# Kernel optimization log

Measured on AMD Instinct MI355X. Metric: run time of the kernel, lower is better.

The kernel has to match this reference:

```python
import jax, jax.numpy as jnp
import numpy as np

N_NODES = 50000
N_EDGES = 800000
FEAT_DIM = 64


def setup_inputs() -> dict:
    key = jax.random.key(0)
    k1, k2, k3 = jax.random.split(key, 3)
    x = jax.random.normal(k1, (N_NODES, FEAT_DIM), dtype=jnp.float32)
    beta = jnp.ones((1,), dtype=jnp.float32)
    # CSR-equivalent edge list: sorted destination rows + random source columns
    row_index = jnp.sort(jax.random.randint(k2, (N_EDGES,), 0, N_NODES, dtype=jnp.int32))
    col_index = jax.random.randint(k3, (N_EDGES,), 0, N_NODES, dtype=jnp.int32)
    return {"x": x, "beta": beta, "row_index": row_index, "col_index": col_index}


def reference(x, beta, row_index, col_index):
    """AGNN layer: SDDMM edge attention (beta * cosine similarity) over the
    sparse graph, per-row softmax, then sparse neighbor aggregation.
    Equivalent math to mygraph.SDDMM + mygraph.agnn_udf (select_id == 5).
    x: [N, D]; row_index/col_index: [E] edge endpoints (row = destination).
    """
    N = x.shape[0]
    eps = 1e-8
    # L2-normalize node features for cosine similarity
    xn = x * jax.lax.rsqrt(jnp.sum(x * x, axis=-1, keepdims=True) + eps)  # [N, D]
    # SDDMM: attention only on existing edges
    att = beta[0] * jnp.sum(xn[row_index] * xn[col_index], axis=-1)  # [E]
    # Numerically stable segment softmax over each destination row
    m = jax.ops.segment_max(att, row_index, num_segments=N)  # [N]
    m = jnp.where(jnp.isfinite(m), m, 0.0)  # empty rows -> -inf guard
    e = jnp.exp(att - m[row_index])  # [E]
    denom = jax.ops.segment_sum(e, row_index, num_segments=N)  # [N]
    alpha = e / jnp.maximum(denom[row_index], 1e-16)  # [E]
    # Sparse aggregation: out_i = sum_j alpha_ij * x_j
    out = jax.ops.segment_sum(alpha[:, None] * x[col_index], row_index, num_segments=N)
    return out
```

## Files before the change

kernel.cpp:

```cpp
#include <hip/hip_runtime.h>
#include <hip/hip_bf16.h>

#define FEAT 64

__global__ void prep_kernel(const float* __restrict__ x,
                            float* __restrict__ rn,
                            const int* __restrict__ row,
                            int* __restrict__ row_ptr,
                            int N, int E, int normBlocks) {
    if ((int)blockIdx.x < normBlocks) {
        int wid  = blockIdx.x * (blockDim.x >> 6) + (threadIdx.x >> 6);
        int lane = threadIdx.x & 63;
        int g    = lane >> 3;
        int sub  = lane & 7;
        int r    = wid * 8 + g;
        if (r >= N) return;
        const char* xB = (const char*)x;
        uint roff = ((uint)r << 8) + ((uint)sub << 4);
        float4 xa = *reinterpret_cast<const float4*>(xB + roff);
        float4 xb = *reinterpret_cast<const float4*>(xB + roff + 128);
        float q = xa.x*xa.x + xa.y*xa.y + xa.z*xa.z + xa.w*xa.w
                + xb.x*xb.x + xb.y*xb.y + xb.z*xb.z + xb.w*xb.w;
        q += __shfl_xor(q, 1);
        q += __shfl_xor(q, 2);
        q += __shfl_xor(q, 4);
        if (sub == 0) rn[r] = rsqrtf(q + 1e-8f);
    } else {
        int e = (blockIdx.x - normBlocks) * blockDim.x + threadIdx.x;
        if (e >= E) return;
        int curr = row[e];
        if (e == 0) {
            for (int r = 0; r <= curr; ++r) row_ptr[r] = 0;
        } else {
            int prev = row[e - 1];
            for (int r = prev + 1; r <= curr; ++r) row_ptr[r] = e;
        }
        if (e == E - 1) {
            for (int r = curr + 1; r <= N; ++r) row_ptr[r] = E;
        }
    }
}

__global__ void fused_kernel(const float* __restrict__ x,
                             const float* __restrict__ rn,
                             const float* __restrict__ beta,
                             const int* __restrict__ row_ptr,
                             const int* __restrict__ col,
                             float* __restrict__ out, int N) {
    int wid  = blockIdx.x * (blockDim.x >> 6) + (threadIdx.x >> 6);
    int lane = threadIdx.x & 63;
    int g    = lane >> 3;
    int sub  = lane & 7;
    int r    = wid * 8 + g;
    bool rv  = (r < N);

    int start = 0, deg = 0;
    if (rv) {
        start = row_ptr[r];
        deg   = row_ptr[r + 1] - start;
    }

    const char* xB   = (const char*)x;
    uint        subo = (uint)sub << 4;

    int   cols8 = 0;
    float rns8  = 0.f;
    if (sub < deg) {
        cols8 = col[start + sub];
        rns8  = rn[cols8];
    }

    float4 xa = make_float4(0.f, 0.f, 0.f, 0.f);
    float4 xb = make_float4(0.f, 0.f, 0.f, 0.f);
    if (rv) {
        uint roff = ((uint)r << 8) + subo;
        xa = *reinterpret_cast<const float4*>(xB + roff);
        xb = *reinterpret_cast<const float4*>(xB + roff + 128);
        float brn = beta[0] * rn[r];
        xa.x *= brn; xa.y *= brn; xa.z *= brn; xa.w *= brn;
        xb.x *= brn; xb.y *= brn; xb.z *= brn; xb.w *= brn;
    }

    float  s = 0.f;
    float4 aa = make_float4(0.f, 0.f, 0.f, 0.f);
    float4 ab = make_float4(0.f, 0.f, 0.f, 0.f);

    for (int k = 0; k < deg; k += 2) {
        int kk = k & 7;
        if (k && kk == 0) {
            if (k + sub < deg) {
                cols8 = col[start + k + sub];
                rns8  = rn[cols8];
            }
        }
        int   c0  = __shfl(cols8, kk, 8);
        float rn0 = __shfl(rns8,  kk, 8);
        int   c1  = __shfl(cols8, kk + 1, 8);
        float rn1 = __shfl(rns8,  kk + 1, 8);
        bool  v1  = (k + 1) < deg;

        uint o0 = ((uint)c0 << 8) + subo;
        float4 va0 = *reinterpret_cast<const float4*>(xB + o0);
        float4 vb0 = *reinterpret_cast<const float4*>(xB + o0 + 128);
        float4 va1 = make_float4(0.f, 0.f, 0.f, 0.f);
        float4 vb1 = make_float4(0.f, 0.f, 0.f, 0.f);
        if (v1) {
            uint o1 = ((uint)c1 << 8) + subo;
            va1 = *reinterpret_cast<const float4*>(xB + o1);
            vb1 = *reinterpret_cast<const float4*>(xB + o1 + 128);
        }

        float d0 = xa.x*va0.x + xa.y*va0.y + xa.z*va0.z + xa.w*va0.w
                 + xb.x*vb0.x + xb.y*vb0.y + xb.z*vb0.z + xb.w*vb0.w;
        float d1 = xa.x*va1.x + xa.y*va1.y + xa.z*va1.z + xa.w*va1.w
                 + xb.x*vb1.x + xb.y*vb1.y + xb.z*vb1.z + xb.w*vb1.w;
        d0 += __shfl_xor(d0, 1);  d1 += __shfl_xor(d1, 1);
        d0 += __shfl_xor(d0, 2);  d1 += __shfl_xor(d1, 2);
        d0 += __shfl_xor(d0, 4);  d1 += __shfl_xor(d1, 4);

        float e0 = __expf(d0 * rn0);
        float e1 = v1 ? __expf(d1 * rn1) : 0.f;
        s += e0 + e1;

        aa.x += e0 * va0.x + e1 * va1.x;  aa.y += e0 * va0.y + e1 * va1.y;
        aa.z += e0 * va0.z + e1 * va1.z;  aa.w += e0 * va0.w + e1 * va1.w;
        ab.x += e0 * vb0.x + e1 * vb1.x;  ab.y += e0 * vb0.y + e1 * vb1.y;
        ab.z += e0 * vb0.z + e1 * vb1.z;  ab.w += e0 * vb0.w + e1 * vb1.w;
    }

    float inv = 1.0f / fmaxf(s, 1e-16f);
    if (rv) {
        uint roff = ((uint)r << 8) + subo;
        *reinterpret_cast<float4*>((char*)out + roff) =
            make_float4(aa.x * inv, aa.y * inv, aa.z * inv, aa.w * inv);
        *reinterpret_cast<float4*>((char*)out + roff + 128) =
            make_float4(ab.x * inv, ab.y * inv, ab.z * inv, ab.w * inv);
    }
}

extern "C" void kernel_launch(void* const* d_in, const int* in_sizes, int n_in,
                              void* d_out, int out_size, void* d_ws, size_t ws_size,
                              hipStream_t stream) {
    const float* x    = (const float*)d_in[0];
    const float* beta = (const float*)d_in[1];
    const int*   row  = (const int*)d_in[2];
    const int*   col  = (const int*)d_in[3];
    float*       out  = (float*)d_out;

    const int N = in_sizes[0] / FEAT;
    const int E = in_sizes[2];

    float* rn      = (float*)d_ws;
    int*   row_ptr = (int*)(rn + ((N + 63) & ~63));

    {
        int normBlocks = (N + 31) / 32;
        int edgeBlocks = (E + 255) / 256;
        prep_kernel<<<normBlocks + edgeBlocks, 256, 0, stream>>>(
            x, rn, row, row_ptr, N, E, normBlocks);
    }
    {
        int waves = (N + 7) / 8;
        int grid  = (waves + 3) / 4;
        fused_kernel<<<grid, 256, 0, stream>>>(x, rn, beta, row_ptr, col, out, N);
    }
}
```

Baseline: 41.71 us.

## Gather bf16 normalized features and assign one wave per row

The prep kernel now also writes a bf16 copy of the L2-normalized features plus each row's norm. The fused kernel gathers these 128-byte bf16 rows instead of 256-byte fp32 rows and rescales by the norm to rebuild x for aggregation, halving gather traffic. Work moves from eight rows per wave to one row per wave, with each 8-lane group taking a different neighbor. Column indices are software-prefetched two chunks ahead and partials are reduced across groups at the end. This adds a workspace buffer and extra prep writes, and bf16 rounding lowers the precision of both the attention scores and the aggregated values.

Measured after the change: 43.35 us. +3.9%, slower.

```diff
diff --git a/kernel.cpp b/kernel.cpp
--- a/kernel.cpp
+++ b/kernel.cpp
@@ -3,8 +3,28 @@
 
 #define FEAT 64
 
+__device__ inline uint packbf2(float lo, float hi) {
+    uint ul = __float_as_uint(lo), uh = __float_as_uint(hi);
+    ul += 0x7FFFu + ((ul >> 16) & 1u);
+    uh += 0x7FFFu + ((uh >> 16) & 1u);
+    return (ul >> 16) | (uh & 0xFFFF0000u);
+}
+
+__device__ inline void unpack8(uint4 q, float4& va, float4& vb) {
+    va.x = __uint_as_float(q.x << 16);
+    va.y = __uint_as_float(q.x & 0xFFFF0000u);
+    va.z = __uint_as_float(q.y << 16);
+    va.w = __uint_as_float(q.y & 0xFFFF0000u);
+    vb.x = __uint_as_float(q.z << 16);
+    vb.y = __uint_as_float(q.z & 0xFFFF0000u);
+    vb.z = __uint_as_float(q.w << 16);
+    vb.w = __uint_as_float(q.w & 0xFFFF0000u);
+}
+
 __global__ void prep_kernel(const float* __restrict__ x,
                             float* __restrict__ rn,
+                            float* __restrict__ nrm,
+                            uint4* __restrict__ xhn,
                             const int* __restrict__ row,
                             int* __restrict__ row_ptr,
                             int N, int E, int normBlocks) {
@@ -24,7 +44,15 @@
         q += __shfl_xor(q, 1);
         q += __shfl_xor(q, 2);
         q += __shfl_xor(q, 4);
-        if (sub == 0) rn[r] = rsqrtf(q + 1e-8f);
+        float qe  = q + 1e-8f;
+        float rnr = rsqrtf(qe);
+        if (sub == 0) { rn[r] = rnr; nrm[r] = qe * rnr; }
+        uint4 p;
+        p.x = packbf2(xa.x * rnr, xa.y * rnr);
+        p.y = packbf2(xa.z * rnr, xa.w * rnr);
+        p.z = packbf2(xb.x * rnr, xb.y * rnr);
+        p.w = packbf2(xb.z * rnr, xb.w * rnr);
+        xhn[r * 8 + sub] = p;
     } else {
         int e = (blockIdx.x - normBlocks) * blockDim.x + threadIdx.x;
         if (e >= E) return;
@@ -42,99 +70,106 @@
 }
 
 __global__ void fused_kernel(const float* __restrict__ x,
+                             const uint4* __restrict__ xhn,
                              const float* __restrict__ rn,
+                             const float* __restrict__ nrm,
                              const float* __restrict__ beta,
                              const int* __restrict__ row_ptr,
                              const int* __restrict__ col,
                              float* __restrict__ out, int N) {
-    int wid  = blockIdx.x * (blockDim.x >> 6) + (threadIdx.x >> 6);
+    int wv   = threadIdx.x >> 6;
+    int r    = blockIdx.x * 4 + wv;
+    if (r >= N) return;
     int lane = threadIdx.x & 63;
     int g    = lane >> 3;
     int sub  = lane & 7;
-    int r    = wid * 8 + g;
-    bool rv  = (r < N);
-
-    int start = 0, deg = 0;
-    if (rv) {
-        start = row_ptr[r];
-        deg   = row_ptr[r + 1] - start;
-    }
-
-    const char* xB   = (const char*)x;
-    uint        subo = (uint)sub << 4;
-
-    int   cols8 = 0;
-    float rns8  = 0.f;
-    if (sub < deg) {
-        cols8 = col[start + sub];
-        rns8  = rn[cols8];
-    }
-
-    float4 xa = make_float4(0.f, 0.f, 0.f, 0.f);
-    float4 xb = make_float4(0.f, 0.f, 0.f, 0.f);
-    if (rv) {
-        uint roff = ((uint)r << 8) + subo;
-        xa = *reinterpret_cast<const float4*>(xB + roff);
-        xb = *reinterpret_cast<const float4*>(xB + roff + 128);
-        float brn = beta[0] * rn[r];
-        xa.x *= brn; xa.y *= brn; xa.z *= brn; xa.w *= brn;
-        xb.x *= brn; xb.y *= brn; xb.z *= brn; xb.w *= brn;
-    }
-
-    float  s = 0.f;
+    uint subo = (uint)sub << 4;
+
+    int start = row_ptr[r];
+    int deg   = row_ptr[r + 1] - start;
+
+    uint roff = ((uint)r << 8) + subo;
+    if (deg == 0) {
+        *reinterpret_cast<float4*>((char*)out + roff) =
+            make_float4(0.f, 0.f, 0.f, 0.f);
+        *reinterpret_cast<float4*>((char*)out + roff + 128) =
+            make_float4(0.f, 0.f, 0.f, 0.f);
+        return;
+    }
+
+    const char* xB = (const char*)x;
+    float4 xa = *reinterpret_cast<const float4*>(xB + roff);
+    float4 xb = *reinterpret_cast<const float4*>(xB + roff + 128);
+    float brn = beta[0] * rn[r];
+    xa.x *= brn; xa.y *= brn; xa.z *= brn; xa.w *= brn;
+    xb.x *= brn; xb.y *= brn; xb.z *= brn; xb.w *= brn;
+
+    int last = start + deg - 1;
+    int nch  = (deg + 7) >> 3;
+
+    int   cc0 = col[min(start + sub, last)];
+    float nn0 = nrm[cc0];
+    int   c_cur = __shfl(cc0, g, 8);
+    float n_cur = __shfl(nn0, g, 8);
+    uint4 q_cur = xhn[(uint)c_cur * 8u + sub];
+    int   ccA = 0; float nnA = 0.f;
+    if (nch > 1) {
+        ccA = col[min(start + 8 + sub, last)];
+        nnA = nrm[ccA];
+    }
+
+    float  s  = 0.f;
     float4 aa = make_float4(0.f, 0.f, 0.f, 0.f);
     float4 ab = make_float4(0.f, 0.f, 0.f, 0.f);
 
-    for (int k = 0; k < deg; k += 2) {
-        int kk = k & 7;
-        if (k && kk == 0) {
-            if (k + sub < deg) {
-                cols8 = col[start + k + sub];
-                rns8  = rn[cols8];
-            }
-        }
-        int   c0  = __shfl(cols8, kk, 8);
-        float rn0 = __shfl(rns8,  kk, 8);
-        int   c1  = __shfl(cols8, kk + 1, 8);
-        float rn1 = __shfl(rns8,  kk + 1, 8);
-        bool  v1  = (k + 1) < deg;
-
-        uint o0 = ((uint)c0 << 8) + subo;
-        float4 va0 = *reinterpret_cast<const float4*>(xB + o0);
-        float4 vb0 = *reinterpret_cast<const float4*>(xB + o0 + 128);
-        float4 va1 = make_float4(0.f, 0.f, 0.f, 0.f);
-        float4 vb1 = make_float4(0.f, 0.f, 0.f, 0.f);
-        if (v1) {
-            uint o1 = ((uint)c1 << 8) + subo;
-            va1 = *reinterpret_cast<const float4*>(xB + o1);
-            vb1 = *reinterpret_cast<const float4*>(xB + o1 + 128);
-        }
-
-        float d0 = xa.x*va0.x + xa.y*va0.y + xa.z*va0.z + xa.w*va0.w
-                 + xb.x*vb0.x + xb.y*vb0.y + xb.z*vb0.z + xb.w*vb0.w;
-        float d1 = xa.x*va1.x + xa.y*va1.y + xa.z*va1.z + xa.w*va1.w
-                 + xb.x*vb1.x + xb.y*vb1.y + xb.z*vb1.z + xb.w*vb1.w;
-        d0 += __shfl_xor(d0, 1);  d1 += __shfl_xor(d1, 1);
-        d0 += __shfl_xor(d0, 2);  d1 += __shfl_xor(d1, 2);
-        d0 += __shfl_xor(d0, 4);  d1 += __shfl_xor(d1, 4);
-
-        float e0 = __expf(d0 * rn0);
-        float e1 = v1 ? __expf(d1 * rn1) : 0.f;
-        s += e0 + e1;
-
-        aa.x += e0 * va0.x + e1 * va1.x;  aa.y += e0 * va0.y + e1 * va1.y;
-        aa.z += e0 * va0.z + e1 * va1.z;  aa.w += e0 * va0.w + e1 * va1.w;
-        ab.x += e0 * vb0.x + e1 * vb1.x;  ab.y += e0 * vb0.y + e1 * vb1.y;
-        ab.z += e0 * vb0.z + e1 * vb1.z;  ab.w += e0 * vb0.w + e1 * vb1.w;
-    }
-
+    for (int t = 0; t < nch; ++t) {
+        int ccB = 0; float nnB = 0.f;
+        if (t + 2 < nch) {
+            ccB = col[min(start + (t + 2) * 8 + sub, last)];
+            nnB = nrm[ccB];
+        }
+        uint4 q_nxt = q_cur; float n_nxt = n_cur;
+        if (t + 1 < nch) {
+            int cs = __shfl(ccA, g, 8);
+            n_nxt  = __shfl(nnA, g, 8);
+            q_nxt  = xhn[(uint)cs * 8u + sub];
+        }
+        float4 va, vb;
+        unpack8(q_cur, va, vb);
+        float d = xa.x*va.x + xa.y*va.y + xa.z*va.z + xa.w*va.w
+                + xb.x*vb.x + xb.y*vb.y + xb.z*vb.z + xb.w*vb.w;
+        d += __shfl_xor(d, 1);
+        d += __shfl_xor(d, 2);
+        d += __shfl_xor(d, 4);
+
+        bool  valid = (t * 8 + g) < deg;
+        float e = valid ? __expf(d) : 0.f;
+        s += e;
+        float w = e * n_cur;
+        aa.x += w * va.x;  aa.y += w * va.y;
+        aa.z += w * va.z;  aa.w += w * va.w;
+        ab.x += w * vb.x;  ab.y += w * vb.y;
+        ab.z += w * vb.z;  ab.w += w * vb.w;
+
+        q_cur = q_nxt;  n_cur = n_nxt;
+        ccA = ccB;      nnA = nnB;
+    }
+
+    #pragma unroll
+    for (int off = 8; off <= 32; off <<= 1) {
+        s    += __shfl_xor(s, off);
+        aa.x += __shfl_xor(aa.x, off);  aa.y += __shfl_xor(aa.y, off);
+        aa.z += __shfl_xor(aa.z, off);  aa.w += __shfl_xor(aa.w, off);
+        ab.x += __shfl_xor(ab.x, off);  ab.y += __shfl_xor(ab.y, off);
+        ab.z += __shfl_xor(ab.z, off);  ab.w += __shfl_xor(ab.w, off);
+    }
     float inv = 1.0f / fmaxf(s, 1e-16f);
-    if (rv) {
-        uint roff = ((uint)r << 8) + subo;
-        *reinterpret_cast<float4*>((char*)out + roff) =
-            make_float4(aa.x * inv, aa.y * inv, aa.z * inv, aa.w * inv);
-        *reinterpret_cast<float4*>((char*)out + roff + 128) =
-            make_float4(ab.x * inv, ab.y * inv, ab.z * inv, ab.w * inv);
+
+    if (lane < 16) {
+        float4 o = (lane < 8) ? aa : ab;
+        uint ooff = ((uint)r << 8) + ((uint)lane << 4);
+        *reinterpret_cast<float4*>((char*)out + ooff) =
+            make_float4(o.x * inv, o.y * inv, o.z * inv, o.w * inv);
     }
 }
 
@@ -150,18 +185,27 @@
     const int N = in_sizes[0] / FEAT;
     const int E = in_sizes[2];
 
-    float* rn      = (float*)d_ws;
-    int*   row_ptr = (int*)(rn + ((N + 63) & ~63));
+    char*  ws = (char*)d_ws;
+    size_t o  = 0;
+    auto alloc = [&](size_t bytes) {
+        size_t cur = o;
+        o = (o + bytes + 511) & ~(size_t)511;
+        return cur;
+    };
+    float* rn      = (float*)(ws + alloc((size_t)N * 4));
+    float* nrm     = (float*)(ws + alloc((size_t)N * 4));
+    int*   row_ptr = (int*)  (ws + alloc((size_t)(N + 1) * 4));
+    uint4* xhn     = (uint4*)(ws + alloc((size_t)N * 128));
 
     {
         int normBlocks = (N + 31) / 32;
         int edgeBlocks = (E + 255) / 256;
         prep_kernel<<<normBlocks + edgeBlocks, 256, 0, stream>>>(
-            x, rn, row, row_ptr, N, E, normBlocks);
+            x, rn, nrm, xhn, row, row_ptr, N, E, normBlocks);
     }
     {
-        int waves = (N + 7) / 8;
-        int grid  = (waves + 3) / 4;
-        fused_kernel<<<grid, 256, 0, stream>>>(x, rn, beta, row_ptr, col, out, N);
-    }
-}
+        int grid = (N + 3) / 4;
+        fused_kernel<<<grid, 256, 0, stream>>>(
+            x, xhn, rn, nrm, beta, row_ptr, col, out, N);
+    }
+}
```
